# Performance work log

Measured on AMD Instinct MI355X. Metric: run time of the kernel, lower is better.

Reference implementation:

```python
import jax, jax.numpy as jnp
import numpy as np


def setup_inputs() -> dict:
    key = jax.random.key(0)
    kx, km = jax.random.split(key)
    B, D, O = 16384, 256, 32
    x = jax.random.normal(kx, (B, D), dtype=jnp.float32)
    M = jax.random.uniform(km, (D, O), dtype=jnp.float32)
    return {"x": x, "M": M}


def reference(x, M):
    # NMU forward: y[b, o] = prod_d (M_hat[d, o] * x[b, d] + 1 - M_hat[d, o])
    M_hat = jnp.clip(M, 0.0, 1.0)                      # [D, O]
    # affine broadcast: [B, D, 1] * [1, D, O] -> [B, D, O]
    t = x[:, :, None] * M_hat[None, :, :] + (1.0 - M_hat)[None, :, :]
    return jnp.prod(t, axis=1)                          # [B, O]
```

## Files before the change

### kernel.cpp

```cpp
#include <hip/hip_runtime.h>


typedef float v2f __attribute__((ext_vector_type(2)));

constexpr int D  = 256;
constexpr int O  = 32;
constexpr int HD = D / 2;
constexpr int ROWS_PW = 8;
constexpr int WAVES   = 4;
constexpr int ROWS_PB = ROWS_PW * WAVES;

__global__ __launch_bounds__(256, 2)
void nmu_fwd(const float* __restrict__ x, const float* __restrict__ M,
             float* __restrict__ y)
{
    const int tid  = threadIdx.x;
    const int lane = tid & 63;
    const int w    = tid >> 6;
    const int o    = lane & 31;
    const int dh   = lane >> 5;
    const int row0 = blockIdx.x * ROWS_PB + w * ROWS_PW;

    v2f m[HD / 2];
    const float* Mp = M + (dh * HD) * O + o;
#pragma unroll
    for (int j = 0; j < HD / 2; ++j) {
        float a = Mp[(2 * j    ) * O];
        float b = Mp[(2 * j + 1) * O];
        m[j].x = __builtin_amdgcn_fmed3f(a, 0.0f, 1.0f);
        m[j].y = __builtin_amdgcn_fmed3f(b, 0.0f, 1.0f);
    }

    const float* xbase = x + dh * HD;

#pragma unroll 1
    for (int r = 0; r < ROWS_PW; ++r) {
        const int row = row0 + r;
        const float4* xp = reinterpret_cast<const float4*>(xbase + row * D);

        float4 cur[8], nxt[8];
#pragma unroll
        for (int u = 0; u < 8; ++u) cur[u] = xp[u];

        v2f p = {1.0f, 1.0f};
#pragma unroll
        for (int c = 0; c < 4; ++c) {
            if (c < 3) {
#pragma unroll
                for (int u = 0; u < 8; ++u) nxt[u] = xp[(c + 1) * 8 + u];
            }
            v2f t[16];
#pragma unroll
            for (int u = 0; u < 8; ++u) {
                const int f = c * 8 + u;
                v2f x01 = {cur[u].x - 1.0f, cur[u].y - 1.0f};
                v2f x23 = {cur[u].z - 1.0f, cur[u].w - 1.0f};
                t[2 * u]     = m[2 * f]     * x01 + (v2f){1.0f, 1.0f};
                t[2 * u + 1] = m[2 * f + 1] * x23 + (v2f){1.0f, 1.0f};
            }
#pragma unroll
            for (int i = 0; i < 8; ++i) t[i] *= t[i + 8];
#pragma unroll
            for (int i = 0; i < 4; ++i) t[i] *= t[i + 4];
            t[0] *= t[2]; t[1] *= t[3];
            p *= t[0] * t[1];
#pragma unroll
            for (int u = 0; u < 8; ++u) cur[u] = nxt[u];
        }

        float s = p.x * p.y;
        s *= __shfl_xor(s, 32, 64);
        if (dh == 0)
            y[row * O + o] = s;
    }
}

extern "C" void kernel_launch(void* const* d_in, const int* in_sizes, int n_in,
                              void* d_out, int out_size, void* d_ws, size_t ws_size,
                              hipStream_t stream) {
    const float* x = (const float*)d_in[0];
    const float* M = (const float*)d_in[1];
    float* y = (float*)d_out;
    const int B = in_sizes[0] / D;
    dim3 grid(B / ROWS_PB);
    nmu_fwd<<<grid, 256, 0, stream>>>(x, M, y);
}
```

Measured before the change: 80.39 us.

## Stage block's x tile in LDS with coalesced loads before compute

Each block now cooperatively loads its whole 32-row x tile into shared memory with fully coalesced float4 loads, syncs once, and then each wave reads its rows from LDS instead of from global memory. The previous per-wave register double-buffered prefetch is removed. The goal is to replace the redundant, broadcast-style global loads (32 lanes reading the same address) with one coalesced read per element. In exchange it adds 32 KB of LDS per block and a barrier, and drops the overlap between loads and compute.

After: 73.06 us. 1.1x faster.

```diff
diff --git a/kernel.cpp b/kernel.cpp
--- a/kernel.cpp
+++ b/kernel.cpp
@@ -9,20 +9,22 @@
 constexpr int ROWS_PW = 8;
 constexpr int WAVES   = 4;
 constexpr int ROWS_PB = ROWS_PW * WAVES;
+constexpr int TILE_F4 = ROWS_PB * D / 4;
 
 __global__ __launch_bounds__(256, 2)
 void nmu_fwd(const float* __restrict__ x, const float* __restrict__ M,
              float* __restrict__ y)
 {
+    __shared__ __align__(16) float xs[ROWS_PB * D];
     const int tid  = threadIdx.x;
     const int lane = tid & 63;
     const int w    = tid >> 6;
     const int o    = lane & 31;
     const int dh   = lane >> 5;
-    const int row0 = blockIdx.x * ROWS_PB + w * ROWS_PW;
+    const int row0 = blockIdx.x * ROWS_PB;
 
+    const float* Mp = M + (dh * HD) * O + o;
     v2f m[HD / 2];
-    const float* Mp = M + (dh * HD) * O + o;
 #pragma unroll
     for (int j = 0; j < HD / 2; ++j) {
         float a = Mp[(2 * j    ) * O];
@@ -31,30 +33,33 @@
         m[j].y = __builtin_amdgcn_fmed3f(b, 0.0f, 1.0f);
     }
 
-    const float* xbase = x + dh * HD;
+    const float4* xg = reinterpret_cast<const float4*>(x + row0 * D);
+    float4* lp = reinterpret_cast<float4*>(xs);
+    float4 st[8];
+#pragma unroll
+    for (int i = 0; i < 8; ++i) st[i] = xg[i * 256 + tid];
+#pragma unroll
+    for (int i = 0; i < 8; ++i) lp[i * 256 + tid] = st[i];
+    __syncthreads();
 
 #pragma unroll 1
     for (int r = 0; r < ROWS_PW; ++r) {
-        const int row = row0 + r;
-        const float4* xp = reinterpret_cast<const float4*>(xbase + row * D);
-
-        float4 cur[8], nxt[8];
-#pragma unroll
-        for (int u = 0; u < 8; ++u) cur[u] = xp[u];
+        const int row = w * ROWS_PW + r;
+        const float4* xr = reinterpret_cast<const float4*>(
+            xs + row * D + dh * HD);
 
         v2f p = {1.0f, 1.0f};
 #pragma unroll
         for (int c = 0; c < 4; ++c) {
-            if (c < 3) {
+            float4 xv[8];
 #pragma unroll
-                for (int u = 0; u < 8; ++u) nxt[u] = xp[(c + 1) * 8 + u];
-            }
+            for (int u = 0; u < 8; ++u) xv[u] = xr[c * 8 + u];
             v2f t[16];
 #pragma unroll
             for (int u = 0; u < 8; ++u) {
                 const int f = c * 8 + u;
-                v2f x01 = {cur[u].x - 1.0f, cur[u].y - 1.0f};
-                v2f x23 = {cur[u].z - 1.0f, cur[u].w - 1.0f};
+                v2f x01 = {xv[u].x - 1.0f, xv[u].y - 1.0f};
+                v2f x23 = {xv[u].z - 1.0f, xv[u].w - 1.0f};
                 t[2 * u]     = m[2 * f]     * x01 + (v2f){1.0f, 1.0f};
                 t[2 * u + 1] = m[2 * f + 1] * x23 + (v2f){1.0f, 1.0f};
             }
@@ -64,14 +69,12 @@
             for (int i = 0; i < 4; ++i) t[i] *= t[i + 4];
             t[0] *= t[2]; t[1] *= t[3];
             p *= t[0] * t[1];
-#pragma unroll
-            for (int u = 0; u < 8; ++u) cur[u] = nxt[u];
         }
 
         float s = p.x * p.y;
         s *= __shfl_xor(s, 32, 64);
         if (dh == 0)
-            y[row * O + o] = s;
+            y[(row0 + row) * O + o] = s;
     }
 }
 
```

## Split the reduction dimension into quarters across wave pairs and combine in shared memory

Applied to the files above, without the earlier changes.

Each wave now covers a quarter of the D dimension instead of half, so it holds 64 clamped M values in registers rather than 128. Rows per block drop to 16, which doubles the grid, and the launch bound asks for 4 blocks per CU. Partial products go to padded shared memory and are multiplied together after a block barrier, then written out as float4 stores. The aim is to cut register pressure and raise occupancy and latency hiding, at the cost of a shared-memory reduction step and a barrier.

Result: slower. 113.1 us (+40.7%).

```diff
diff --git a/kernel.cpp b/kernel.cpp
--- a/kernel.cpp
+++ b/kernel.cpp
@@ -3,75 +3,93 @@
 
 typedef float v2f __attribute__((ext_vector_type(2)));
 
-constexpr int D  = 256;
-constexpr int O  = 32;
-constexpr int HD = D / 2;
-constexpr int ROWS_PW = 8;
-constexpr int WAVES   = 4;
-constexpr int ROWS_PB = ROWS_PW * WAVES;
+constexpr int D   = 256;
+constexpr int O   = 32;
+constexpr int QD  = 64;
+constexpr int RPP = 8;
+constexpr int ROWS_PB = 16;
+constexpr int PSTR = 132;
 
-__global__ __launch_bounds__(256, 2)
+__global__ __launch_bounds__(256, 4)
 void nmu_fwd(const float* __restrict__ x, const float* __restrict__ M,
              float* __restrict__ y)
 {
+    __shared__ float part[ROWS_PB * PSTR];
     const int tid  = threadIdx.x;
     const int lane = tid & 63;
     const int w    = tid >> 6;
     const int o    = lane & 31;
     const int dh   = lane >> 5;
-    const int row0 = blockIdx.x * ROWS_PB + w * ROWS_PW;
+    const int pair = w >> 1;
+    const int qq   = ((w & 1) << 1) | dh;
+    const int rowbase = blockIdx.x * ROWS_PB + pair * RPP;
 
-    v2f m[HD / 2];
-    const float* Mp = M + (dh * HD) * O + o;
+    const float* Mp = M + qq * QD * O + o;
+    v2f m[QD / 2];
 #pragma unroll
-    for (int j = 0; j < HD / 2; ++j) {
+    for (int j = 0; j < QD / 2; ++j) {
         float a = Mp[(2 * j    ) * O];
         float b = Mp[(2 * j + 1) * O];
         m[j].x = __builtin_amdgcn_fmed3f(a, 0.0f, 1.0f);
         m[j].y = __builtin_amdgcn_fmed3f(b, 0.0f, 1.0f);
     }
 
-    const float* xbase = x + dh * HD;
+    const float4* xg = reinterpret_cast<const float4*>(x);
+    auto saddr = [&](int s) {
+        const int r = s >> 2, c = s & 3;
+        return xg + (size_t)(rowbase + r) * (D / 4) + qq * (QD / 4) + c * 4;
+    };
+    float4 buf[2][4];
+    {
+        const float4* a0 = saddr(0);
+#pragma unroll
+        for (int u = 0; u < 4; ++u) buf[0][u] = a0[u];
+    }
 
-#pragma unroll 1
-    for (int r = 0; r < ROWS_PW; ++r) {
-        const int row = row0 + r;
-        const float4* xp = reinterpret_cast<const float4*>(xbase + row * D);
+    v2f p = {1.0f, 1.0f};
+#pragma unroll 4
+    for (int s = 0; s < RPP * 4; ++s) {
+        if (s + 1 < RPP * 4) {
+            const float4* an = saddr(s + 1);
+#pragma unroll
+            for (int u = 0; u < 4; ++u) buf[(s + 1) & 1][u] = an[u];
+        }
+        v2f acc;
+#pragma unroll
+        for (int u = 0; u < 4; ++u) {
+            const float4 xv = buf[s & 1][u];
+            const int f = (s & 3) * 4 + u;
+            v2f x01 = {xv.x - 1.0f, xv.y - 1.0f};
+            v2f x23 = {xv.z - 1.0f, xv.w - 1.0f};
+            v2f t0 = m[2 * f]     * x01 + (v2f){1.0f, 1.0f};
+            v2f t1 = m[2 * f + 1] * x23 + (v2f){1.0f, 1.0f};
+            v2f q = t0 * t1;
+            acc = (u == 0) ? q : acc * q;
+        }
+        p *= acc;
+        if ((s & 3) == 3) {
+            const int br = pair * RPP + (s >> 2);
+            part[br * PSTR + qq * O + o] = p.x * p.y;
+            p = (v2f){1.0f, 1.0f};
+        }
+    }
+    __syncthreads();
 
-        float4 cur[8], nxt[8];
-#pragma unroll
-        for (int u = 0; u < 8; ++u) cur[u] = xp[u];
-
-        v2f p = {1.0f, 1.0f};
-#pragma unroll
-        for (int c = 0; c < 4; ++c) {
-            if (c < 3) {
-#pragma unroll
-                for (int u = 0; u < 8; ++u) nxt[u] = xp[(c + 1) * 8 + u];
-            }
-            v2f t[16];
-#pragma unroll
-            for (int u = 0; u < 8; ++u) {
-                const int f = c * 8 + u;
-                v2f x01 = {cur[u].x - 1.0f, cur[u].y - 1.0f};
-                v2f x23 = {cur[u].z - 1.0f, cur[u].w - 1.0f};
-                t[2 * u]     = m[2 * f]     * x01 + (v2f){1.0f, 1.0f};
-                t[2 * u + 1] = m[2 * f + 1] * x23 + (v2f){1.0f, 1.0f};
-            }
-#pragma unroll
-            for (int i = 0; i < 8; ++i) t[i] *= t[i + 8];
-#pragma unroll
-            for (int i = 0; i < 4; ++i) t[i] *= t[i + 4];
-            t[0] *= t[2]; t[1] *= t[3];
-            p *= t[0] * t[1];
-#pragma unroll
-            for (int u = 0; u < 8; ++u) cur[u] = nxt[u];
-        }
-
-        float s = p.x * p.y;
-        s *= __shfl_xor(s, 32, 64);
-        if (dh == 0)
-            y[row * O + o] = s;
+    if (tid < ROWS_PB * 8) {
+        const int r  = tid >> 3;
+        const int o4 = tid & 7;
+        const float* pb = &part[r * PSTR + o4 * 4];
+        float4 a = *reinterpret_cast<const float4*>(pb);
+        float4 b = *reinterpret_cast<const float4*>(pb + O);
+        float4 c = *reinterpret_cast<const float4*>(pb + 2 * O);
+        float4 d = *reinterpret_cast<const float4*>(pb + 3 * O);
+        float4 out;
+        out.x = a.x * b.x * c.x * d.x;
+        out.y = a.y * b.y * c.y * d.y;
+        out.z = a.z * b.z * c.z * d.z;
+        out.w = a.w * b.w * c.w * d.w;
+        *reinterpret_cast<float4*>(
+            y + (blockIdx.x * ROWS_PB + r) * O + o4 * 4) = out;
     }
 }
 
```
